# Kernel tuning notes

Measured on AMD Instinct MI355X. Metric: run time of the kernel, lower is better.

The kernel has to match this reference:

```python
import jax, jax.numpy as jnp
import numpy as np

NEG_INF = -1e20

def setup_inputs() -> dict:
    key = jax.random.key(0)
    kq, kk, kv, km = jax.random.split(key, 4)
    B, S, H, D = 2, 2048, 16, 64
    queries = jax.random.normal(kq, (B, S, H, D), dtype=jnp.float32)
    keys = jax.random.normal(kk, (B, S, H, D), dtype=jnp.float32)
    values = jax.random.normal(kv, (B, S, H, D), dtype=jnp.float32)
    mask = jax.random.randint(km, (B, 1, 1, S), 0, 2, dtype=jnp.int32)
    return {"queries": queries, "keys": keys, "values": values, "mask": mask}

def reference(queries, keys, values, mask):
    # scores: [B, H, Q, K]
    dk = keys.shape[-1]
    scores = jnp.einsum('bqhd,bkhd->bhqk', queries, keys) / jnp.sqrt(jnp.asarray(dk, queries.dtype))
    scores = jnp.where(mask == 0, jnp.asarray(NEG_INF, scores.dtype), scores)
    attn = jax.nn.softmax(scores, axis=-1)
    # dropout p=0.0 (eval): identity
    out = jnp.einsum('bhqv,bvhd->bqhd', attn, values)
    return out
```

## Files before the change

kernel.cpp:

```cpp
#include <hip/hip_runtime.h>
#include <hip/hip_bf16.h>

#define S_LEN 2048
#define NH 16
#define HD 64
#define KT_N 32

typedef __attribute__((ext_vector_type(8))) __bf16 bf16x8;
typedef __attribute__((ext_vector_type(4))) float f32x4;
typedef __attribute__((ext_vector_type(16))) float f32x16;

#define QSCALE 0.1803368801111204f

static __device__ __forceinline__ ushort f2bf(float f) {
    unsigned int u = __float_as_uint(f);
    u += 0x7fffu + ((u >> 16) & 1u);
    return (ushort)(u >> 16);
}

static __device__ __forceinline__ void gload16(const void* g, void* l) {
    __builtin_amdgcn_global_load_lds(
        (const __attribute__((address_space(1))) unsigned int*)g,
        (__attribute__((address_space(3))) unsigned int*)l, 16, 0, 0);
}
static __device__ __forceinline__ void gload4(const void* g, void* l) {
    __builtin_amdgcn_global_load_lds(
        (const __attribute__((address_space(1))) unsigned int*)g,
        (__attribute__((address_space(3))) unsigned int*)l, 4, 0, 0);
}

static __device__ __forceinline__ unsigned cvtpk_bf16(float lo, float hi) {
    unsigned r;
    asm("v_cvt_pk_bf16_f32 %0, %1, %2" : "=v"(r) : "v"(lo), "v"(hi));
    return r;
}
static __device__ __forceinline__ float exp2_fast(float x) {
    float r;
    asm("v_exp_f32 %0, %1" : "=v"(r) : "v"(x));
    return r;
}

__global__ __launch_bounds__(256) void prep_k_kernel(const float* __restrict__ in,
                                                     ushort* __restrict__ out) {
    unsigned t = blockIdx.x * 256u + threadIdx.x;
    unsigned o = t & 7u;
    unsigned s = (t >> 3) & 2047u;
    unsigned bh = t >> 14;
    unsigned b = bh >> 4, h = bh & 15u;
    const float* src = in + (((size_t)(b * S_LEN) + s) * NH + h) * HD + o * 8;
    float4 x = *(const float4*)src;
    float4 y = *(const float4*)(src + 4);
    union { ushort u[8]; uint4 q; } fu;
    fu.u[0] = f2bf(x.x); fu.u[1] = f2bf(x.y); fu.u[2] = f2bf(x.z); fu.u[3] = f2bf(x.w);
    fu.u[4] = f2bf(y.x); fu.u[5] = f2bf(y.y); fu.u[6] = f2bf(y.z); fu.u[7] = f2bf(y.w);
    unsigned kt = s >> 6, kh = (s >> 5) & 1u, kl = s & 31u;
    unsigned dchunk = o >> 1, ho = o & 1u;
    size_t ci = (((size_t)(bh * 32u + kt) * 2u + kh) * 4u + dchunk) * 64u + kl + 32u * ho;
    *(uint4*)(out + ci * 8u) = fu.q;
}

__global__ __launch_bounds__(256) void prep_v_kernel(const float* __restrict__ in,
                                                     ushort* __restrict__ out) {
    __shared__ float T[64][68];
    const unsigned tid = threadIdx.x;
    const unsigned kt = blockIdx.x, bh = blockIdx.y;
    const unsigned b = bh >> 4, h = bh & 15u;
#pragma unroll
    for (int i = 0; i < 4; ++i) {
        unsigned idx = tid + i * 256u;
        unsigned sl = idx >> 4, d4 = (idx & 15u) * 4u;
        float4 v = *(const float4*)(in + (((size_t)(b * S_LEN) + kt * 64u + sl) * NH + h) * HD + d4);
        *(float4*)&T[sl][d4] = v;
    }
    __syncthreads();
#pragma unroll
    for (int it = 0; it < 2; ++it) {
        unsigned ct = tid + it * 256u;
        unsigned l = ct & 63u, sub = ct >> 6;
        unsigned nt = sub & 1u, c = (sub >> 1) & 1u, kh = sub >> 2;
        unsigned d = (l & 31u) + 32u * nt;
        unsigned kb = kh * 32u + c * 16u + (l >> 5) * 8u;
        union { ushort u[8]; uint4 q; } fu;
#pragma unroll
        for (int j = 0; j < 8; ++j) fu.u[j] = f2bf(T[kb + j][d]);
        *(uint4*)(out + ((size_t)(bh * 32u + kt) * 8u + sub) * 512u + l * 8u) = fu.q;
    }
}

__global__ __launch_bounds__(256) void attn_kernel(const float* __restrict__ Qp,
                                                   const ushort* __restrict__ Kws,
                                                   const ushort* __restrict__ Vws,
                                                   const int* __restrict__ maskp,
                                                   float* __restrict__ outp) {
    __shared__ ushort Kbuf[2][4096];
    __shared__ ushort Vbuf[2][4096];
    __shared__ int    mbuf[2][64];
    __shared__ float  rls[4][32];

    const unsigned tid = threadIdx.x;
    const unsigned wid = tid >> 6;
    const unsigned lane = tid & 63u;
    const unsigned l31 = lane & 31u;
    const unsigned hi = lane >> 5;

    const unsigned bh = blockIdx.y;
    const unsigned b = bh >> 4, h = bh & 15u;
    const unsigned q0 = blockIdx.x * 128u + wid * 32u;

    bf16x8 qf[4];
    {
        const float* qb = Qp + (((size_t)(b * S_LEN) + q0 + l31) * NH + h) * HD + hi * 8u;
#pragma unroll
        for (int dc = 0; dc < 4; ++dc) {
            float4 x = *(const float4*)(qb + dc * 16);
            float4 y = *(const float4*)(qb + dc * 16 + 4);
            union { ushort u[8]; bf16x8 v; } fu;
            fu.u[0] = f2bf(x.x * QSCALE); fu.u[1] = f2bf(x.y * QSCALE);
            fu.u[2] = f2bf(x.z * QSCALE); fu.u[3] = f2bf(x.w * QSCALE);
            fu.u[4] = f2bf(y.x * QSCALE); fu.u[5] = f2bf(y.y * QSCALE);
            fu.u[6] = f2bf(y.z * QSCALE); fu.u[7] = f2bf(y.w * QSCALE);
            qf[dc] = fu.v;
        }
    }

    f32x16 oacc0 = {0,0,0,0,0,0,0,0,0,0,0,0,0,0,0,0};
    f32x16 oacc1 = {0,0,0,0,0,0,0,0,0,0,0,0,0,0,0,0};
    float lsum = 0.f;

    const char* kbase_g = (const char*)Kws + (size_t)bh * 262144u;
    const char* vbase_g = (const char*)Vws + (size_t)bh * 262144u;
    const int* mb_g = maskp + (size_t)b * S_LEN;

#define STAGE(KT, PB) do {                                                        \
    unsigned seg0 = 2u * wid;                                                     \
    gload16(kbase_g + ((size_t)(KT) * 8u + seg0) * 1024u + lane * 16u,            \
            &Kbuf[PB][seg0 * 512u]);                                              \
    gload16(kbase_g + ((size_t)(KT) * 8u + seg0 + 1u) * 1024u + lane * 16u,       \
            &Kbuf[PB][(seg0 + 1u) * 512u]);                                       \
    gload16(vbase_g + ((size_t)(KT) * 8u + seg0) * 1024u + lane * 16u,            \
            &Vbuf[PB][seg0 * 512u]);                                              \
    gload16(vbase_g + ((size_t)(KT) * 8u + seg0 + 1u) * 1024u + lane * 16u,       \
            &Vbuf[PB][(seg0 + 1u) * 512u]);                                       \
    if (wid == 0) gload4(mb_g + (KT) * 64 + lane, &mbuf[PB][0]);                  \
  } while (0)

    STAGE(0, 0);
    asm volatile("s_waitcnt vmcnt(0)" ::: "memory");
    __syncthreads();

    unsigned pb = 0;
    for (int kt = 0; kt < KT_N; ++kt) {
        if (kt < KT_N - 1) STAGE(kt + 1, pb ^ 1u);

#pragma unroll
        for (int kh = 0; kh < 2; ++kh) {
            bf16x8 kf[4];
#pragma unroll
            for (int dc = 0; dc < 4; ++dc)
                kf[dc] = *(const bf16x8*)&Kbuf[pb][(kh * 4 + dc) * 512u + lane * 8u];
            f32x16 s = {0,0,0,0,0,0,0,0,0,0,0,0,0,0,0,0};
#pragma unroll
            for (int dc = 0; dc < 4; ++dc)
                s = __builtin_amdgcn_mfma_f32_32x32x16_bf16(kf[dc], qf[dc], s, 0, 0, 0);

            float p[16];
#pragma unroll
            for (int r1 = 0; r1 < 4; ++r1) {
                int mv[4];
                *(int4*)mv = *(const int4*)&mbuf[pb][kh * 32 + r1 * 8 + hi * 4];
#pragma unroll
                for (int r0 = 0; r0 < 4; ++r0) {
                    const int reg = r1 * 4 + r0;
                    float t = mv[r0] ? s[reg] : -1e30f;
                    float e = exp2_fast(t);
                    p[reg] = e;
                    lsum += e;
                }
            }

#pragma unroll
            for (int c = 0; c < 2; ++c) {
                unsigned x  = cvtpk_bf16(p[8 * c + 0], p[8 * c + 1]);
                unsigned x2 = cvtpk_bf16(p[8 * c + 2], p[8 * c + 3]);
                unsigned y  = cvtpk_bf16(p[8 * c + 4], p[8 * c + 5]);
                unsigned y2 = cvtpk_bf16(p[8 * c + 6], p[8 * c + 7]);
                unsigned xs  = (unsigned)__shfl_xor((int)x, 32);
                unsigned x2s = (unsigned)__shfl_xor((int)x2, 32);
                unsigned ys  = (unsigned)__shfl_xor((int)y, 32);
                unsigned y2s = (unsigned)__shfl_xor((int)y2, 32);
                union { unsigned w[4]; bf16x8 v; } pa;
                pa.w[0] = hi ? ys  : x;
                pa.w[1] = hi ? y2s : x2;
                pa.w[2] = hi ? y   : xs;
                pa.w[3] = hi ? y2  : x2s;
#pragma unroll
                for (int nt = 0; nt < 2; ++nt) {
                    bf16x8 vf = *(const bf16x8*)
                        &Vbuf[pb][((kh * 2 + c) * 2 + nt) * 512u + lane * 8u];
                    if (nt == 0)
                        oacc0 = __builtin_amdgcn_mfma_f32_32x32x16_bf16(pa.v, vf, oacc0, 0, 0, 0);
                    else
                        oacc1 = __builtin_amdgcn_mfma_f32_32x32x16_bf16(pa.v, vf, oacc1, 0, 0, 0);
                }
            }
        }
        asm volatile("s_waitcnt vmcnt(0)" ::: "memory");
        __syncthreads();
        pb ^= 1u;
    }
#undef STAGE

    lsum += __shfl_xor(lsum, 32);
    if (hi == 0) rls[wid][l31] = 1.0f / lsum;
    __syncthreads();

#pragma unroll
    for (int r1 = 0; r1 < 4; ++r1) {
#pragma unroll
        for (int r0 = 0; r0 < 4; ++r0) {
            const int reg = r1 * 4 + r0;
            const unsigned q = r0 + 8u * r1 + 4u * hi;
            const float rr = rls[wid][q];
            float* ob = outp + (((size_t)(b * S_LEN) + q0 + q) * NH + h) * HD + l31;
            ob[0]  = oacc0[reg] * rr;
            ob[32] = oacc1[reg] * rr;
        }
    }
}

extern "C" void kernel_launch(void* const* d_in, const int* in_sizes, int n_in,
                              void* d_out, int out_size, void* d_ws, size_t ws_size,
                              hipStream_t stream) {
    const float* Qp = (const float*)d_in[0];
    const float* Kp = (const float*)d_in[1];
    const float* Vp = (const float*)d_in[2];
    const int* maskp = (const int*)d_in[3];
    float* outp = (float*)d_out;

    ushort* Kws = (ushort*)d_ws;
    ushort* Vws = Kws + (size_t)2 * NH * S_LEN * HD;

    hipLaunchKernelGGL(prep_k_kernel, dim3(2048), dim3(256), 0, stream, Kp, Kws);
    hipLaunchKernelGGL(prep_v_kernel, dim3(KT_N, 32), dim3(256), 0, stream, Vp, Vws);
    hipLaunchKernelGGL(attn_kernel, dim3(S_LEN / 128, 32), dim3(256), 0, stream,
                       Qp, Kws, Vws, maskp, outp);
}
```

Measured before the change: 78.00 us.

## Triple-buffer K/V staging with partial vmcnt waits and MFMA priority hints

Replaces the double-buffered K/V/mask LDS pipeline with a three-stage ring, so loads run two tiles ahead. The full vmcnt(0) drain before each barrier becomes a partial vmcnt(4) wait, and __syncthreads becomes a raw s_barrier. The aim is to hide global-load latency behind the MFMA work on the current tile. It also wraps the MFMA groups in s_setprio, splits the row-sum into four independent accumulators, and adds an occupancy hint of 2 blocks per CU. The cost is 50% more LDS and correctness that depends on exact per-wave load counts, since wave 0 issues one extra mask load per stage.

New measurement: 76.38 us. 2.1% less time.

```diff
diff --git a/kernel.cpp b/kernel.cpp
--- a/kernel.cpp
+++ b/kernel.cpp
@@ -7,7 +7,6 @@
 #define KT_N 32
 
 typedef __attribute__((ext_vector_type(8))) __bf16 bf16x8;
-typedef __attribute__((ext_vector_type(4))) float f32x4;
 typedef __attribute__((ext_vector_type(16))) float f32x16;
 
 #define QSCALE 0.1803368801111204f
@@ -87,14 +86,14 @@
     }
 }
 
-__global__ __launch_bounds__(256) void attn_kernel(const float* __restrict__ Qp,
-                                                   const ushort* __restrict__ Kws,
-                                                   const ushort* __restrict__ Vws,
-                                                   const int* __restrict__ maskp,
-                                                   float* __restrict__ outp) {
-    __shared__ ushort Kbuf[2][4096];
-    __shared__ ushort Vbuf[2][4096];
-    __shared__ int    mbuf[2][64];
+__global__ __launch_bounds__(256, 2) void attn_kernel(const float* __restrict__ Qp,
+                                                      const ushort* __restrict__ Kws,
+                                                      const ushort* __restrict__ Vtb,
+                                                      const int* __restrict__ maskp,
+                                                      float* __restrict__ outp) {
+    __shared__ __align__(16) ushort Kbuf[3][4096];
+    __shared__ __align__(16) ushort Vbuf[3][4096];
+    __shared__ __align__(16) int    mbuf[3][64];
     __shared__ float  rls[4][32];
 
     const unsigned tid = threadIdx.x;
@@ -125,10 +124,10 @@
 
     f32x16 oacc0 = {0,0,0,0,0,0,0,0,0,0,0,0,0,0,0,0};
     f32x16 oacc1 = {0,0,0,0,0,0,0,0,0,0,0,0,0,0,0,0};
-    float lsum = 0.f;
+    float ls0 = 0.f, ls1 = 0.f, ls2 = 0.f, ls3 = 0.f;
 
     const char* kbase_g = (const char*)Kws + (size_t)bh * 262144u;
-    const char* vbase_g = (const char*)Vws + (size_t)bh * 262144u;
+    const char* vbase_g = (const char*)Vtb + (size_t)bh * 262144u;
     const int* mb_g = maskp + (size_t)b * S_LEN;
 
 #define STAGE(KT, PB) do {                                                        \
@@ -144,38 +143,45 @@
     if (wid == 0) gload4(mb_g + (KT) * 64 + lane, &mbuf[PB][0]);                  \
   } while (0)
 
-    STAGE(0, 0);
-    asm volatile("s_waitcnt vmcnt(0)" ::: "memory");
-    __syncthreads();
-
-    unsigned pb = 0;
-    for (int kt = 0; kt < KT_N; ++kt) {
-        if (kt < KT_N - 1) STAGE(kt + 1, pb ^ 1u);
+    STAGE(0, 0u);
+    STAGE(1, 1u);
+    asm volatile("s_waitcnt vmcnt(4)" ::: "memory");
+    __builtin_amdgcn_s_barrier();
+
+    unsigned cur = 0u, st = 2u;
+    for (int i = 0; i < KT_N; ++i) {
+        if (i < KT_N - 2) STAGE(i + 2, st);
+        const ushort* kr = &Kbuf[cur][0];
+        const ushort* vr = &Vbuf[cur][0];
+        const int*    mr = &mbuf[cur][0];
 
 #pragma unroll
         for (int kh = 0; kh < 2; ++kh) {
             bf16x8 kf[4];
 #pragma unroll
             for (int dc = 0; dc < 4; ++dc)
-                kf[dc] = *(const bf16x8*)&Kbuf[pb][(kh * 4 + dc) * 512u + lane * 8u];
+                kf[dc] = *(const bf16x8*)&kr[(kh * 4 + dc) * 512u + lane * 8u];
+
             f32x16 s = {0,0,0,0,0,0,0,0,0,0,0,0,0,0,0,0};
+            __builtin_amdgcn_s_setprio(1);
 #pragma unroll
             for (int dc = 0; dc < 4; ++dc)
                 s = __builtin_amdgcn_mfma_f32_32x32x16_bf16(kf[dc], qf[dc], s, 0, 0, 0);
+            __builtin_amdgcn_s_setprio(0);
 
             float p[16];
 #pragma unroll
             for (int r1 = 0; r1 < 4; ++r1) {
                 int mv[4];
-                *(int4*)mv = *(const int4*)&mbuf[pb][kh * 32 + r1 * 8 + hi * 4];
+                *(int4*)mv = *(const int4*)&mr[kh * 32 + r1 * 8 + hi * 4];
 #pragma unroll
                 for (int r0 = 0; r0 < 4; ++r0) {
                     const int reg = r1 * 4 + r0;
                     float t = mv[r0] ? s[reg] : -1e30f;
-                    float e = exp2_fast(t);
-                    p[reg] = e;
-                    lsum += e;
+                    p[reg] = exp2_fast(t);
                 }
+                ls0 += p[r1 * 4 + 0]; ls1 += p[r1 * 4 + 1];
+                ls2 += p[r1 * 4 + 2]; ls3 += p[r1 * 4 + 3];
             }
 
 #pragma unroll
@@ -193,23 +199,24 @@
                 pa.w[1] = hi ? y2s : x2;
                 pa.w[2] = hi ? y   : xs;
                 pa.w[3] = hi ? y2  : x2s;
-#pragma unroll
-                for (int nt = 0; nt < 2; ++nt) {
-                    bf16x8 vf = *(const bf16x8*)
-                        &Vbuf[pb][((kh * 2 + c) * 2 + nt) * 512u + lane * 8u];
-                    if (nt == 0)
-                        oacc0 = __builtin_amdgcn_mfma_f32_32x32x16_bf16(pa.v, vf, oacc0, 0, 0, 0);
-                    else
-                        oacc1 = __builtin_amdgcn_mfma_f32_32x32x16_bf16(pa.v, vf, oacc1, 0, 0, 0);
-                }
+                bf16x8 vf0 = *(const bf16x8*)&vr[((kh * 2 + c) * 2 + 0) * 512u + lane * 8u];
+                bf16x8 vf1 = *(const bf16x8*)&vr[((kh * 2 + c) * 2 + 1) * 512u + lane * 8u];
+                __builtin_amdgcn_s_setprio(1);
+                oacc0 = __builtin_amdgcn_mfma_f32_32x32x16_bf16(pa.v, vf0, oacc0, 0, 0, 0);
+                oacc1 = __builtin_amdgcn_mfma_f32_32x32x16_bf16(pa.v, vf1, oacc1, 0, 0, 0);
+                __builtin_amdgcn_s_setprio(0);
             }
         }
-        asm volatile("s_waitcnt vmcnt(0)" ::: "memory");
-        __syncthreads();
-        pb ^= 1u;
+
+        if (i < KT_N - 2) asm volatile("s_waitcnt vmcnt(4)" ::: "memory");
+        else              asm volatile("s_waitcnt vmcnt(0)" ::: "memory");
+        __builtin_amdgcn_s_barrier();
+        cur = (cur == 2u) ? 0u : cur + 1u;
+        st  = (st  == 2u) ? 0u : st  + 1u;
     }
 #undef STAGE
 
+    float lsum = (ls0 + ls1) + (ls2 + ls3);
     lsum += __shfl_xor(lsum, 32);
     if (hi == 0) rls[wid][l31] = 1.0f / lsum;
     __syncthreads();
```
